# Optimization experiments

Measured on AMD Instinct MI355X. Metric: run time of the kernel, lower is better.

Reference implementation:

```python
import jax, jax.numpy as jnp
import numpy as np

B, Q, C, NH, DH = 16, 300, 256, 8, 32
SPATIAL = [(80, 80), (40, 40), (20, 20), (10, 10)]
NPTS = [4, 4, 4, 4]
SUMP = sum(NPTS)
OFFSET_SCALE = 0.5


def _grid_bias():
    # directional init from build(): unit directions per head, scaled 1..n per level
    thetas = np.arange(NH) * (2.0 * np.pi / NH)
    g = np.stack([np.cos(thetas), np.sin(thetas)], -1)
    g = g / np.abs(g).max(-1, keepdims=True)
    g = np.tile(g[:, None, :], (1, SUMP, 1))
    scal = np.concatenate([np.arange(1, n + 1) for n in NPTS])[None, :, None]
    return (g * scal).astype(np.float32)


def setup_inputs() -> dict:
    key = jax.random.key(0)
    ks = jax.random.split(key, 5)
    S = sum(h * w for h, w in SPATIAL)
    return {
        "hidden_states": jax.random.normal(ks[0], (B, Q, C), jnp.float32),
        "encoder_hidden_states": jax.random.normal(ks[1], (B, S, C), jnp.float32),
        "reference_points": jax.random.uniform(ks[2], (B, Q, 1, 4), jnp.float32),
        "off_kernel": jax.random.normal(ks[3], (C, NH, SUMP, 2), jnp.float32) * 0.01,
        "off_bias": jnp.asarray(_grid_bias()),
        "attn_kernel": jax.random.normal(ks[4], (C, NH, SUMP), jnp.float32) * 0.01,
        "attn_bias": jnp.zeros((NH, SUMP), jnp.float32),
        "num_points_scale": jnp.asarray(
            np.concatenate([np.full(n, 1.0 / n) for n in NPTS]).astype(np.float32)
        ),
        "spatial_shapes": jnp.asarray(SPATIAL, jnp.int32),
    }


def _bilinear(v, loc, H, W):
    # v: [B, NH, H*W, DH]; loc: [B, Q, NH, P, 2] normalized in [0,1]
    # grid_sample(bilinear, align_corners=False, zeros padding) on grid 2*loc-1
    x = loc[..., 0] * W - 0.5
    y = loc[..., 1] * H - 0.5
    x0 = jnp.floor(x)
    y0 = jnp.floor(y)
    lx = x - x0
    ly = y - y0
    x0i = x0.astype(jnp.int32)
    y0i = y0.astype(jnp.int32)
    Bv = v.shape[0]
    Ql, Pl = loc.shape[1], loc.shape[3]
    out = jnp.zeros((Bv, NH, Ql, Pl, DH), v.dtype)
    corners = ((0, 0, (1 - lx) * (1 - ly)), (1, 0, lx * (1 - ly)),
               (0, 1, (1 - lx) * ly), (1, 1, lx * ly))
    for dx, dy, w in corners:
        xc = x0i + dx
        yc = y0i + dy
        valid = (xc >= 0) & (xc < W) & (yc >= 0) & (yc < H)
        idx = jnp.clip(yc, 0, H - 1) * W + jnp.clip(xc, 0, W - 1)  # [B,Q,NH,P]
        idx_t = jnp.transpose(idx, (0, 2, 1, 3)).reshape(Bv, NH, Ql * Pl, 1)
        g = jnp.take_along_axis(v, idx_t, axis=2).reshape(Bv, NH, Ql, Pl, DH)
        wt = (w * valid).astype(v.dtype)  # [B,Q,NH,P]
        out = out + g * jnp.transpose(wt, (0, 2, 1, 3))[..., None]
    return out  # [B,NH,Q,P,DH]


def reference(hidden_states, encoder_hidden_states, reference_points, off_kernel,
              off_bias, attn_kernel, attn_bias, num_points_scale, spatial_shapes):
    # sampling offsets / attention weights projections (EinsumDense equivalents)
    offsets = jnp.einsum('bqc,chpt->bqhpt', hidden_states, off_kernel) + off_bias
    attn = jax.nn.softmax(
        jnp.einsum('bqc,chp->bqhp', hidden_states, attn_kernel) + attn_bias, axis=-1)
    # 4-d reference points branch: center + scaled offsets * box wh
    center = jnp.expand_dims(reference_points[..., :2], -2)   # [B,Q,1,1,2]
    wh = jnp.expand_dims(reference_points[..., 2:], -2)       # [B,Q,1,1,2]
    loc = center + offsets * num_points_scale[:, None] * wh * OFFSET_SCALE  # [B,Q,NH,SUMP,2]
    S = encoder_hidden_states.shape[1]
    value = encoder_hidden_states.reshape(B, S, NH, DH).transpose(0, 2, 1, 3)  # [B,NH,S,DH]
    out = jnp.zeros((B, Q, NH, DH), hidden_states.dtype)
    start, pstart = 0, 0
    for (H, W), P in zip(SPATIAL, NPTS):
        v = value[:, :, start:start + H * W, :]
        l = loc[:, :, :, pstart:pstart + P, :]
        sampled = _bilinear(v, l, H, W)  # [B,NH,Q,P,DH]
        out = out + jnp.einsum('bhqpd,bqhp->bqhd', sampled,
                               attn[:, :, :, pstart:pstart + P])
        start += H * W
        pstart += P
    return out.reshape(B, Q, C), attn
```

## Files before the change

kernel.cpp:

```cpp
#include <hip/hip_runtime.h>
#include <math.h>

#define BB 16
#define QQ 300
#define CC 256
#define NHH 8
#define DHH 32
#define SUMPP 16
#define SSS 8500
#define GQ 10
#define QT (QQ / GQ)

__global__ __launch_bounds__(384) void precompute_kernel(
    const float* __restrict__ hs,
    const float* __restrict__ refp,
    const float* __restrict__ off_k,
    const float* __restrict__ off_b,
    const float* __restrict__ attn_k,
    const float* __restrict__ attn_b,
    const float* __restrict__ nps,
    float* __restrict__ loc_t,
    float* __restrict__ aw_t,
    float* __restrict__ attn_out)
{
    const int t = threadIdx.x;
    const int blk = blockIdx.x;
    const int b = blk / QT;
    const int q0 = (blk % QT) * GQ;
    const float* hsb = hs + ((size_t)b * QQ + q0) * CC;

    float acc[GQ];
#pragma unroll
    for (int g = 0; g < GQ; ++g) acc[g] = 0.f;

    if (t < 256) {
        const int h = t >> 5;
        const int p = (t >> 1) & 15;
        const int xy = t & 1;
        const float* kcol = off_k + t;
#pragma unroll 8
        for (int c = 0; c < CC; ++c) {
            const float k = kcol[c * 256];
#pragma unroll
            for (int g = 0; g < GQ; ++g)
                acc[g] = fmaf(hsb[g * CC + c], k, acc[g]);
        }
        const float scale = nps[p] * 0.5f;
        const float bias = off_b[t];
        const int didx = ((p * 8 + h) << 1) | xy;
#pragma unroll
        for (int g = 0; g < GQ; ++g) {
            const float4 r = *(const float4*)(refp + ((size_t)b * QQ + q0 + g) * 4);
            const float center = xy ? r.y : r.x;
            const float wh     = xy ? r.w : r.z;
            loc_t[((size_t)b * QQ + q0 + g) * 256 + didx] =
                fmaf((acc[g] + bias) * scale, wh, center);
        }
    } else {
        const int j = t - 256;
        const int h = j >> 4;
        const int p = j & 15;
        const float* kcol = attn_k + j;
#pragma unroll 8
        for (int c = 0; c < CC; ++c) {
            const float k = kcol[c * 128];
#pragma unroll
            for (int g = 0; g < GQ; ++g)
                acc[g] = fmaf(hsb[g * CC + c], k, acc[g]);
        }
        const float bias = attn_b[j];
#pragma unroll
        for (int g = 0; g < GQ; ++g) {
            const float logit = acc[g] + bias;
            float m = logit;
#pragma unroll
            for (int o = 1; o < 16; o <<= 1)
                m = fmaxf(m, __shfl_xor(m, o));
            const float e = __expf(logit - m);
            float s = e;
#pragma unroll
            for (int o = 1; o < 16; o <<= 1)
                s += __shfl_xor(s, o);
            const float a = e / s;
            attn_out[((size_t)b * QQ + q0 + g) * 128 + j] = a;
            aw_t[((size_t)b * QQ + q0 + g) * 128 + p * 8 + h] = a;
        }
    }
}

__global__ __launch_bounds__(256) void sample_kernel(
    const float* __restrict__ enc,
    const float2* __restrict__ loc2,
    const float* __restrict__ aw_t,
    float* __restrict__ out)
{
    __shared__ float2 sh_l[4 * 128];
    __shared__ float  sh_a[4 * 128];

    const int g = blockIdx.x;
    const int xcd = g & 7;
    const int i = g >> 3;
    const int b = ((i & 1) << 3) | xcd;
    const int q0 = (i >> 1) * 4;
    const size_t qbase = (size_t)b * QQ + q0;

    const int t = threadIdx.x;
    const float2* lsrc = loc2 + qbase * 128;
    sh_l[t] = lsrc[t];
    sh_l[t + 256] = lsrc[t + 256];
    const float* asrc = aw_t + qbase * 128;
    sh_a[t] = asrc[t];
    sh_a[t + 256] = asrc[t + 256];
    __syncthreads();

    const int qs = t >> 6;
    const int lane = t & 63;
    const int h = lane >> 3;
    const int d4 = (lane & 7) << 2;
    const float* vb = enc + (size_t)b * SSS * 256 + h * 32 + d4;

    float4 acc = {0.f, 0.f, 0.f, 0.f};

    const int HWs[4]    = {80, 40, 20, 10};
    const int starts[4] = {0, 6400, 8000, 8400};

    int p = 0;
#pragma unroll
    for (int lvl = 0; lvl < 4; ++lvl) {
        const int Wd = HWs[lvl];
        const float Wf = (float)Wd;
        const int st = starts[lvl];
#pragma unroll
        for (int pp = 0; pp < 4; ++pp, ++p) {
            const float2 l = sh_l[qs * 128 + p * 8 + h];
            const float  a = sh_a[qs * 128 + p * 8 + h];

            const float x = l.x * Wf - 0.5f;
            const float y = l.y * Wf - 0.5f;
            const float x0f = floorf(x), y0f = floorf(y);
            const float lx = x - x0f, ly = y - y0f;
            const int x0 = (int)x0f, y0 = (int)y0f;
            const int x1 = x0 + 1, y1 = y0 + 1;

            const bool vx0 = (unsigned)x0 < (unsigned)Wd;
            const bool vx1 = (unsigned)x1 < (unsigned)Wd;
            const bool vy0 = (unsigned)y0 < (unsigned)Wd;
            const bool vy1 = (unsigned)y1 < (unsigned)Wd;

            const int x0c = min(max(x0, 0), Wd - 1);
            const int x1c = min(max(x1, 0), Wd - 1);
            const int y0c = min(max(y0, 0), Wd - 1);
            const int y1c = min(max(y1, 0), Wd - 1);

            float w00 = (1.f - lx) * (1.f - ly) * a;
            float w10 = lx * (1.f - ly) * a;
            float w01 = (1.f - lx) * ly * a;
            float w11 = lx * ly * a;
            w00 = (vx0 & vy0) ? w00 : 0.f;
            w10 = (vx1 & vy0) ? w10 : 0.f;
            w01 = (vx0 & vy1) ? w01 : 0.f;
            w11 = (vx1 & vy1) ? w11 : 0.f;

            const float* r0 = vb + (size_t)(st + y0c * Wd) * 256;
            const float* r1 = vb + (size_t)(st + y1c * Wd) * 256;
            const float4 v00 = *(const float4*)(r0 + ((size_t)x0c << 8));
            const float4 v10 = *(const float4*)(r0 + ((size_t)x1c << 8));
            const float4 v01 = *(const float4*)(r1 + ((size_t)x0c << 8));
            const float4 v11 = *(const float4*)(r1 + ((size_t)x1c << 8));

            acc.x = fmaf(w00, v00.x, fmaf(w10, v10.x, fmaf(w01, v01.x, fmaf(w11, v11.x, acc.x))));
            acc.y = fmaf(w00, v00.y, fmaf(w10, v10.y, fmaf(w01, v01.y, fmaf(w11, v11.y, acc.y))));
            acc.z = fmaf(w00, v00.z, fmaf(w10, v10.z, fmaf(w01, v01.z, fmaf(w11, v11.z, acc.z))));
            acc.w = fmaf(w00, v00.w, fmaf(w10, v10.w, fmaf(w01, v01.w, fmaf(w11, v11.w, acc.w))));
        }
    }

    float* op = out + (qbase + qs) * 256 + h * 32 + d4;
    *(float4*)op = acc;
}

extern "C" void kernel_launch(void* const* d_in, const int* in_sizes, int n_in,
                              void* d_out, int out_size, void* d_ws, size_t ws_size,
                              hipStream_t stream) {
    const float* hs     = (const float*)d_in[0];
    const float* enc    = (const float*)d_in[1];
    const float* refp   = (const float*)d_in[2];
    const float* off_k  = (const float*)d_in[3];
    const float* off_b  = (const float*)d_in[4];
    const float* attn_k = (const float*)d_in[5];
    const float* attn_b = (const float*)d_in[6];
    const float* nps    = (const float*)d_in[7];

    float* out      = (float*)d_out;
    float* attn_out = out + (size_t)BB * QQ * CC;
    float* loc_t    = (float*)d_ws;
    float* aw_t     = loc_t + (size_t)BB * QQ * 256;

    precompute_kernel<<<BB * QT, 384, 0, stream>>>(hs, refp, off_k, off_b,
                                                   attn_k, attn_b, nps,
                                                   loc_t, aw_t, attn_out);
    sample_kernel<<<BB * (QQ / 4), 256, 0, stream>>>(enc, (const float2*)loc_t,
                                                     aw_t, out);
}
```

Baseline: 244.4 us.

## Split sampling points across two wavefronts per query and reduce in shared memory

The sample kernel now handles two queries per block instead of four, and the 16 sampling points of each query are split between two wavefronts that each do 8 points. The partial sums are then combined through shared memory. Location and attention weight are packed into one float4 in shared memory, and the address arithmetic uses 32-bit integers. The aim is twice as many blocks and a shorter serial gather chain per thread, exposing more memory-level parallelism. The cost is an extra barrier, a shared-memory reduction, and half the threads sitting idle during the final store.

Measured after the change: 243.5 us. About the same (-0.4%).

```diff
diff --git a/kernel.cpp b/kernel.cpp
--- a/kernel.cpp
+++ b/kernel.cpp
@@ -94,89 +94,94 @@
     const float* __restrict__ aw_t,
     float* __restrict__ out)
 {
-    __shared__ float2 sh_l[4 * 128];
-    __shared__ float  sh_a[4 * 128];
+    __shared__ float4 sh[2 * 128];
+    __shared__ float4 sh_red[128];
 
     const int g = blockIdx.x;
     const int xcd = g & 7;
     const int i = g >> 3;
     const int b = ((i & 1) << 3) | xcd;
-    const int q0 = (i >> 1) * 4;
-    const size_t qbase = (size_t)b * QQ + q0;
+    const int q0 = (i >> 1) * 2;
+    const int qbase = b * QQ + q0;
 
     const int t = threadIdx.x;
-    const float2* lsrc = loc2 + qbase * 128;
-    sh_l[t] = lsrc[t];
-    sh_l[t + 256] = lsrc[t + 256];
-    const float* asrc = aw_t + qbase * 128;
-    sh_a[t] = asrc[t];
-    sh_a[t + 256] = asrc[t + 256];
+    {
+        const float2 l = loc2[(size_t)qbase * 128 + t];
+        const float  a = aw_t[(size_t)qbase * 128 + t];
+        sh[t] = make_float4(l.x, l.y, a, 0.f);
+    }
     __syncthreads();
 
-    const int qs = t >> 6;
+    const int qs = t >> 7;
+    const int pw = (t >> 6) & 1;
     const int lane = t & 63;
     const int h = lane >> 3;
     const int d4 = (lane & 7) << 2;
-    const float* vb = enc + (size_t)b * SSS * 256 + h * 32 + d4;
+    const float* vb = enc + b * (SSS * 256) + h * 32 + d4;
 
     float4 acc = {0.f, 0.f, 0.f, 0.f};
 
     const int HWs[4]    = {80, 40, 20, 10};
     const int starts[4] = {0, 6400, 8000, 8400};
 
-    int p = 0;
-#pragma unroll
-    for (int lvl = 0; lvl < 4; ++lvl) {
+#pragma unroll
+    for (int j = 0; j < 8; ++j) {
+        const int lvl = j >> 1;
+        const int p = 2 * j + pw;
         const int Wd = HWs[lvl];
         const float Wf = (float)Wd;
         const int st = starts[lvl];
-#pragma unroll
-        for (int pp = 0; pp < 4; ++pp, ++p) {
-            const float2 l = sh_l[qs * 128 + p * 8 + h];
-            const float  a = sh_a[qs * 128 + p * 8 + h];
-
-            const float x = l.x * Wf - 0.5f;
-            const float y = l.y * Wf - 0.5f;
-            const float x0f = floorf(x), y0f = floorf(y);
-            const float lx = x - x0f, ly = y - y0f;
-            const int x0 = (int)x0f, y0 = (int)y0f;
-            const int x1 = x0 + 1, y1 = y0 + 1;
-
-            const bool vx0 = (unsigned)x0 < (unsigned)Wd;
-            const bool vx1 = (unsigned)x1 < (unsigned)Wd;
-            const bool vy0 = (unsigned)y0 < (unsigned)Wd;
-            const bool vy1 = (unsigned)y1 < (unsigned)Wd;
-
-            const int x0c = min(max(x0, 0), Wd - 1);
-            const int x1c = min(max(x1, 0), Wd - 1);
-            const int y0c = min(max(y0, 0), Wd - 1);
-            const int y1c = min(max(y1, 0), Wd - 1);
-
-            float w00 = (1.f - lx) * (1.f - ly) * a;
-            float w10 = lx * (1.f - ly) * a;
-            float w01 = (1.f - lx) * ly * a;
-            float w11 = lx * ly * a;
-            w00 = (vx0 & vy0) ? w00 : 0.f;
-            w10 = (vx1 & vy0) ? w10 : 0.f;
-            w01 = (vx0 & vy1) ? w01 : 0.f;
-            w11 = (vx1 & vy1) ? w11 : 0.f;
-
-            const float* r0 = vb + (size_t)(st + y0c * Wd) * 256;
-            const float* r1 = vb + (size_t)(st + y1c * Wd) * 256;
-            const float4 v00 = *(const float4*)(r0 + ((size_t)x0c << 8));
-            const float4 v10 = *(const float4*)(r0 + ((size_t)x1c << 8));
-            const float4 v01 = *(const float4*)(r1 + ((size_t)x0c << 8));
-            const float4 v11 = *(const float4*)(r1 + ((size_t)x1c << 8));
-
-            acc.x = fmaf(w00, v00.x, fmaf(w10, v10.x, fmaf(w01, v01.x, fmaf(w11, v11.x, acc.x))));
-            acc.y = fmaf(w00, v00.y, fmaf(w10, v10.y, fmaf(w01, v01.y, fmaf(w11, v11.y, acc.y))));
-            acc.z = fmaf(w00, v00.z, fmaf(w10, v10.z, fmaf(w01, v01.z, fmaf(w11, v11.z, acc.z))));
-            acc.w = fmaf(w00, v00.w, fmaf(w10, v10.w, fmaf(w01, v01.w, fmaf(w11, v11.w, acc.w))));
-        }
-    }
-
-    float* op = out + (qbase + qs) * 256 + h * 32 + d4;
-    *(float4*)op = acc;
+
+        const float4 lpa = sh[qs * 128 + p * 8 + h];
+        const float a = lpa.z;
+
+        const float x = lpa.x * Wf - 0.5f;
+        const float y = lpa.y * Wf - 0.5f;
+        const float x0f = floorf(x), y0f = floorf(y);
+        const float lx = x - x0f, ly = y - y0f;
+        const int x0 = (int)x0f, y0 = (int)y0f;
+        const int x1 = x0 + 1, y1 = y0 + 1;
+
+        const bool vx0 = (unsigned)x0 < (unsigned)Wd;
+        const bool vx1 = (unsigned)x1 < (unsigned)Wd;
+        const bool vy0 = (unsigned)y0 < (unsigned)Wd;
+        const bool vy1 = (unsigned)y1 < (unsigned)Wd;
+
+        const int x0c = min(max(x0, 0), Wd - 1);
+        const int x1c = min(max(x1, 0), Wd - 1);
+        const int y0c = min(max(y0, 0), Wd - 1);
+        const int y1c = min(max(y1, 0), Wd - 1);
+
+        float w00 = (1.f - lx) * (1.f - ly) * a;
+        float w10 = lx * (1.f - ly) * a;
+        float w01 = (1.f - lx) * ly * a;
+        float w11 = lx * ly * a;
+        w00 = (vx0 & vy0) ? w00 : 0.f;
+        w10 = (vx1 & vy0) ? w10 : 0.f;
+        w01 = (vx0 & vy1) ? w01 : 0.f;
+        w11 = (vx1 & vy1) ? w11 : 0.f;
+
+        const int r0 = (st + y0c * Wd) << 8;
+        const int r1 = (st + y1c * Wd) << 8;
+        const float4 v00 = *(const float4*)(vb + r0 + (x0c << 8));
+        const float4 v10 = *(const float4*)(vb + r0 + (x1c << 8));
+        const float4 v01 = *(const float4*)(vb + r1 + (x0c << 8));
+        const float4 v11 = *(const float4*)(vb + r1 + (x1c << 8));
+
+        acc.x = fmaf(w00, v00.x, fmaf(w10, v10.x, fmaf(w01, v01.x, fmaf(w11, v11.x, acc.x))));
+        acc.y = fmaf(w00, v00.y, fmaf(w10, v10.y, fmaf(w01, v01.y, fmaf(w11, v11.y, acc.y))));
+        acc.z = fmaf(w00, v00.z, fmaf(w10, v10.z, fmaf(w01, v01.z, fmaf(w11, v11.z, acc.z))));
+        acc.w = fmaf(w00, v00.w, fmaf(w10, v10.w, fmaf(w01, v01.w, fmaf(w11, v11.w, acc.w))));
+    }
+
+    if (pw == 1) sh_red[qs * 64 + lane] = acc;
+    __syncthreads();
+    if (pw == 0) {
+        const float4 o = sh_red[qs * 64 + lane];
+        acc.x += o.x; acc.y += o.y; acc.z += o.z; acc.w += o.w;
+        float* op = out + (size_t)(qbase + qs) * 256 + h * 32 + d4;
+        *(float4*)op = acc;
+    }
 }
 
 extern "C" void kernel_launch(void* const* d_in, const int* in_sizes, int n_in,
@@ -199,6 +204,6 @@
     precompute_kernel<<<BB * QT, 384, 0, stream>>>(hs, refp, off_k, off_b,
                                                    attn_k, attn_b, nps,
                                                    loc_t, aw_t, attn_out);
-    sample_kernel<<<BB * (QQ / 4), 256, 0, stream>>>(enc, (const float2*)loc_t,
+    sample_kernel<<<BB * (QQ / 2), 256, 0, stream>>>(enc, (const float2*)loc_t,
                                                      aw_t, out);
 }
```
